# Optimization experiments

Hardware: AMD Instinct MI355X
Metric: run time of the kernel (lower is better)

Reference implementation:

```python
import jax, jax.numpy as jnp
import numpy as np

N, E, D, ED, H = 50000, 800000, 128, 16, 1
EPS = 1e-5


def setup_inputs() -> dict:
    key = jax.random.key(0)
    ks = jax.random.split(key, 12)
    return {
        "x": jax.random.normal(ks[0], (N, D), jnp.float32),
        "edge_index": jax.random.randint(ks[1], (2, E), 0, N),
        "edge_attr": jax.random.normal(ks[2], (E, ED), jnp.float32),
        # GATv2Conv params
        "W_l": jax.random.normal(ks[3], (D, H * D), jnp.float32) / np.sqrt(D),
        "b_l": jnp.zeros((H * D,), jnp.float32),
        "W_r": jax.random.normal(ks[4], (D, H * D), jnp.float32) / np.sqrt(D),
        "b_r": jnp.zeros((H * D,), jnp.float32),
        "W_e": jax.random.normal(ks[5], (ED, H * D), jnp.float32) / np.sqrt(ED),
        "att": jax.random.normal(ks[6], (H, D), jnp.float32) * 0.1,
        "bias_gat": jnp.zeros((D,), jnp.float32),
        # block params
        "weight1": jax.random.normal(ks[7], (2,), jnp.float32),
        "bn1_gamma": jnp.ones((D,), jnp.float32),
        "bn1_beta": jnp.zeros((D,), jnp.float32),
        "conv_w": jax.random.normal(ks[8], (D, D, 3), jnp.float32) / np.sqrt(3 * D),
        "conv_b": jnp.zeros((D,), jnp.float32),
        "weight2": jax.random.normal(ks[9], (2,), jnp.float32),
        "bn2_gamma": jnp.ones((D,), jnp.float32),
        "bn2_beta": jnp.zeros((D,), jnp.float32),
    }


def _batch_norm(z, gamma, beta):
    # NodeLevelBatchNorm in training mode: stats over all nodes of the batch graph
    mu = z.mean(axis=0)
    var = z.var(axis=0)
    return (z - mu) * jax.lax.rsqrt(var + EPS) * gamma + beta


def _gatv2(x, edge_index, edge_attr, W_l, b_l, W_r, b_r, W_e, att, bias_gat):
    n = x.shape[0]
    # add self loops with edge_attr fill_value=0
    loop = jnp.arange(n)
    src = jnp.concatenate([edge_index[0], loop])  # message sources j
    dst = jnp.concatenate([edge_index[1], loop])  # message targets i
    x_l = (x @ W_l + b_l).reshape(n, H, D)
    x_r = (x @ W_r + b_r).reshape(n, H, D)
    e = (edge_attr @ W_e).reshape(-1, H, D)
    e = jnp.concatenate([e, jnp.zeros((n, H, D), e.dtype)], axis=0)  # zeros: lin_edge(0)=0
    # [E+N, H, D] edge messages
    m = jax.nn.leaky_relu(x_l[src] + x_r[dst] + e, negative_slope=0.2)
    logits = jnp.einsum('ehc,hc->eh', m, att)  # [E+N, H]
    # softmax grouped by target node (every node has a self loop -> no empty segments)
    lmax = jax.ops.segment_max(logits, dst, num_segments=n)
    p = jnp.exp(logits - lmax[dst])
    denom = jax.ops.segment_sum(p, dst, num_segments=n)
    alpha = p / denom[dst]
    out = jax.ops.segment_sum(alpha[:, :, None] * x_l[src], dst, num_segments=n)  # [N,H,D]
    return out.mean(axis=1) + bias_gat  # concat=False -> head mean


def reference(x, edge_index, edge_attr, W_l, b_l, W_r, b_r, W_e, att, bias_gat,
              weight1, bn1_gamma, bn1_beta, conv_w, conv_b, weight2,
              bn2_gamma, bn2_beta):
    attn_feat = _gatv2(x, edge_index, edge_attr, W_l, b_l, W_r, b_r, W_e, att, bias_gat)
    w1 = jax.nn.softmax(weight1)
    z = w1[0] * x + w1[1] * attn_feat
    z = _batch_norm(z, bn1_gamma, bn1_beta)
    # Conv1d over the node dimension: [1, C, N] -> [1, C, N]
    z1 = jax.lax.conv_general_dilated(
        z.T[None], conv_w, window_strides=(1,), padding=[(1, 1)],
        dimension_numbers=('NCH', 'OIH', 'NCH'))
    z1 = z1[0].T + conv_b  # [N, C]
    z1 = jax.nn.leaky_relu(z1, negative_slope=0.01)  # dropout inactive in eval
    w2 = jax.nn.softmax(weight2)
    z = w2[0] * z + w2[1] * z1
    z = _batch_norm(z, bn2_gamma, bn2_beta)
    return z
```

## Files before the change

kernel.cpp:

```cpp
#include <hip/hip_runtime.h>
#include <hip/hip_bf16.h>
#include <math.h>

#define DD 128
#define EPSBN 1e-5f

typedef float f2 __attribute__((ext_vector_type(2)));

__device__ __forceinline__ float4 f4_add(float4 a, float4 b) {
    return make_float4(a.x + b.x, a.y + b.y, a.z + b.z, a.w + b.w);
}
__device__ __forceinline__ float4 f4_fma(float a, float4 b, float4 c) {
    c.x = fmaf(a, b.x, c.x); c.y = fmaf(a, b.y, c.y);
    c.z = fmaf(a, b.z, c.z); c.w = fmaf(a, b.w, c.w);
    return c;
}
__device__ __forceinline__ float leakyf(float v, float s) { return v > 0.f ? v : s * v; }

__device__ __forceinline__ unsigned short f2bf(float f) {
    unsigned u = __float_as_uint(f);
    return (unsigned short)((u + 0x7fffu + ((u >> 16) & 1u)) >> 16);
}
__device__ __forceinline__ f2 bfu2f2(unsigned u) {
    f2 r;
    r.x = __uint_as_float(u << 16);
    r.y = __uint_as_float(u & 0xFFFF0000u);
    return r;
}
__device__ __forceinline__ f2 leaky2(f2 v, float s) {
    f2 z = (f2)0.f;
    return __builtin_elementwise_max(v, z) + s * __builtin_elementwise_min(v, z);
}

__global__ __launch_bounds__(256) void k_prep(const float* __restrict__ conv_w, float* __restrict__ wT,
                                              int* __restrict__ counts, float* __restrict__ stats,
                                              int n, int nstats) {
    int idx = blockIdx.x * 256 + threadIdx.x;
    if (idx < 3 * 128 * 128) {
        int k = idx >> 14;
        int r = idx & 16383;
        int ci = r >> 7, co = r & 127;
        wT[idx] = conv_w[(size_t)co * 384 + ci * 3 + k];
    }
    int z = idx - 3 * 128 * 128;
    if (z >= 0) {
        if (z < n) counts[z] = 0;
        else if (z - n < nstats) stats[z - n] = 0.f;
    }
}

__global__ __launch_bounds__(256) void k_gemm_xlxr(
    const float* __restrict__ x, const float* __restrict__ Wl, const float* __restrict__ bl,
    const float* __restrict__ Wr, const float* __restrict__ br,
    float* __restrict__ XR, unsigned short* __restrict__ XLh, int n)
{
    __shared__ float As[64 * 33];
    __shared__ float Bs[32 * 256];
    int tid = threadIdx.x;
    int r0 = blockIdx.x * 64;
    int tx = tid & 31, ty = tid >> 5;

    float4 accL[8], accR[8];
    #pragma unroll
    for (int j = 0; j < 8; ++j) {
        accL[j] = make_float4(0.f, 0.f, 0.f, 0.f);
        accR[j] = make_float4(0.f, 0.f, 0.f, 0.f);
    }

    for (int k0 = 0; k0 < 128; k0 += 32) {
        for (int idx = tid; idx < 64 * 32; idx += 256) {
            int lrow = idx >> 5, kk = idx & 31;
            int g = r0 + lrow;
            As[lrow * 33 + kk] = (g < n) ? x[(size_t)g * DD + k0 + kk] : 0.f;
        }
        for (int idx = tid; idx < 2048; idx += 256) {
            int kk = idx >> 6, co4 = idx & 63;
            float4 v;
            if (co4 < 32) v = ((const float4*)Wl)[(size_t)(k0 + kk) * 32 + co4];
            else          v = ((const float4*)Wr)[(size_t)(k0 + kk) * 32 + (co4 - 32)];
            ((float4*)Bs)[kk * 64 + co4] = v;
        }
        __syncthreads();

        #pragma unroll 4
        for (int kk = 0; kk < 32; ++kk) {
            float a[8];
            #pragma unroll
            for (int j = 0; j < 8; ++j) a[j] = As[(ty * 8 + j) * 33 + kk];
            float4 bL = ((float4*)Bs)[kk * 64 + tx];
            float4 bR = ((float4*)Bs)[kk * 64 + 32 + tx];
            #pragma unroll
            for (int j = 0; j < 8; ++j) {
                accL[j] = f4_fma(a[j], bL, accL[j]);
                accR[j] = f4_fma(a[j], bR, accR[j]);
            }
        }
        __syncthreads();
    }

    float4 blv = ((const float4*)bl)[tx];
    float4 brv = ((const float4*)br)[tx];
    #pragma unroll
    for (int j = 0; j < 8; ++j) {
        int row = r0 + ty * 8 + j;
        if (row < n) {
            float4 L4 = f4_add(accL[j], blv);
            ((float4*)(XR + (size_t)row * DD))[tx] = f4_add(accR[j], brv);
            uint2 hp;
            hp.x = (unsigned)f2bf(L4.x) | ((unsigned)f2bf(L4.y) << 16);
            hp.y = (unsigned)f2bf(L4.z) | ((unsigned)f2bf(L4.w) << 16);
            ((uint2*)(XLh + (size_t)row * DD))[tx] = hp;
        }
    }
}

__global__ __launch_bounds__(256) void k_hist(const int* __restrict__ dst, int* __restrict__ counts, int e) {
    int idx = blockIdx.x * 256 + threadIdx.x;
    if (idx < e) atomicAdd(&counts[dst[idx]], 1);
}

__global__ __launch_bounds__(256) void k_scan1(const int* __restrict__ counts,
                                               int* __restrict__ offsets, int* __restrict__ bsum, int n) {
    __shared__ int tmp[256];
    int t = threadIdx.x;
    int i = blockIdx.x * 256 + t;
    int v = (i < n) ? counts[i] : 0;
    tmp[t] = v;
    __syncthreads();
    for (int off = 1; off < 256; off <<= 1) {
        int u = (t >= off) ? tmp[t - off] : 0;
        __syncthreads();
        tmp[t] += u;
        __syncthreads();
    }
    if (i < n) offsets[i] = tmp[t] - v;
    if (t == 255) bsum[blockIdx.x] = tmp[255];
}

__global__ __launch_bounds__(1024) void k_scan2(int* __restrict__ bsum, int nchunks) {
    __shared__ int tmp[1024];
    int t = threadIdx.x;
    int v = (t < nchunks) ? bsum[t] : 0;
    tmp[t] = v;
    __syncthreads();
    for (int off = 1; off < 1024; off <<= 1) {
        int u = (t >= off) ? tmp[t - off] : 0;
        __syncthreads();
        tmp[t] += u;
        __syncthreads();
    }
    if (t < nchunks) bsum[t] = tmp[t] - v;
    if (t == 0) bsum[nchunks] = tmp[nchunks - 1];
}

__global__ __launch_bounds__(256) void k_scan3(int* __restrict__ offsets, int* __restrict__ cursor,
                                               const int* __restrict__ bsum, int n, int nchunks) {
    int i = blockIdx.x * 256 + threadIdx.x;
    if (i < n) {
        int o = offsets[i] + bsum[i >> 8];
        offsets[i] = o;
        cursor[i] = o;
    }
    if (i == n) offsets[n] = bsum[nchunks];
}

__global__ __launch_bounds__(256) void k_scatter(const int* __restrict__ src, const int* __restrict__ dst,
                                                 int* __restrict__ cursor, int2* __restrict__ epair, int e) {
    int idx = blockIdx.x * 256 + threadIdx.x;
    if (idx >= e) return;
    int d = dst[idx];
    int pos = atomicAdd(&cursor[d], 1);
    epair[pos] = make_int2(idx, src[idx]);
}


#define EPROJ(EB_, J_, EV_) {                                                   \
    const float4* e4_ = ((const float4*)(EB_)) + (J_) * 4;                      \
    float4 a0_ = e4_[0], a1_ = e4_[1], a2_ = e4_[2], a3_ = e4_[3];              \
    f2 v_ = (f2)0.f;                                                            \
    v_ = __builtin_elementwise_fma((f2)a0_.x, w2[0],  v_);                      \
    v_ = __builtin_elementwise_fma((f2)a0_.y, w2[1],  v_);                      \
    v_ = __builtin_elementwise_fma((f2)a0_.z, w2[2],  v_);                      \
    v_ = __builtin_elementwise_fma((f2)a0_.w, w2[3],  v_);                      \
    v_ = __builtin_elementwise_fma((f2)a1_.x, w2[4],  v_);                      \
    v_ = __builtin_elementwise_fma((f2)a1_.y, w2[5],  v_);                      \
    v_ = __builtin_elementwise_fma((f2)a1_.z, w2[6],  v_);                      \
    v_ = __builtin_elementwise_fma((f2)a1_.w, w2[7],  v_);                      \
    v_ = __builtin_elementwise_fma((f2)a2_.x, w2[8],  v_);                      \
    v_ = __builtin_elementwise_fma((f2)a2_.y, w2[9],  v_);                      \
    v_ = __builtin_elementwise_fma((f2)a2_.z, w2[10], v_);                      \
    v_ = __builtin_elementwise_fma((f2)a2_.w, w2[11], v_);                      \
    v_ = __builtin_elementwise_fma((f2)a3_.x, w2[12], v_);                      \
    v_ = __builtin_elementwise_fma((f2)a3_.y, w2[13], v_);                      \
    v_ = __builtin_elementwise_fma((f2)a3_.z, w2[14], v_);                      \
    v_ = __builtin_elementwise_fma((f2)a3_.w, w2[15], v_);                      \
    EV_ = v_; }

#define GAT_LOAD4(q_, U0_, U1_, U2_, U3_, AV_) {                                \
    int2 g0_ = epair[q_], g1_ = epair[(q_) + 1];                                \
    int2 g2_ = epair[(q_) + 2], g3_ = epair[(q_) + 3];                          \
    int s0_ = __builtin_amdgcn_readfirstlane(g0_.y);                            \
    int s1_ = __builtin_amdgcn_readfirstlane(g1_.y);                            \
    int s2_ = __builtin_amdgcn_readfirstlane(g2_.y);                            \
    int s3_ = __builtin_amdgcn_readfirstlane(g3_.y);                            \
    U0_ = XLu[(size_t)s0_ * 64 + lane];                                         \
    U1_ = XLu[(size_t)s1_ * 64 + lane];                                         \
    U2_ = XLu[(size_t)s2_ * 64 + lane];                                         \
    U3_ = XLu[(size_t)s3_ * 64 + lane];                                         \
    int ej_ = esel == 0 ? g0_.x : esel == 1 ? g1_.x : esel == 2 ? g2_.x : g3_.x;\
    AV_ = edge_attr[(size_t)ej_ * 16 + ek]; }

#define GAT_COMPUTE4(U0_, U1_, U2_, U3_, EB_) {                                 \
    f2 x0_ = bfu2f2(U0_), x1_ = bfu2f2(U1_);                                    \
    f2 x2_ = bfu2f2(U2_), x3_ = bfu2f2(U3_);                                    \
    f2 ev0_, ev1_, ev2_, ev3_;                                                  \
    EPROJ(EB_, 0, ev0_); EPROJ(EB_, 1, ev1_);                                   \
    EPROJ(EB_, 2, ev2_); EPROJ(EB_, 3, ev3_);                                   \
    f2 m0_ = leaky2(x0_ + xr2 + ev0_, 0.2f);                                    \
    f2 m1_ = leaky2(x1_ + xr2 + ev1_, 0.2f);                                    \
    f2 m2_ = leaky2(x2_ + xr2 + ev2_, 0.2f);                                    \
    f2 m3_ = leaky2(x3_ + xr2 + ev3_, 0.2f);                                    \
    float l0_ = m0_.x * att2.x + m0_.y * att2.y;                                \
    float l1_ = m1_.x * att2.x + m1_.y * att2.y;                                \
    float l2_ = m2_.x * att2.x + m2_.y * att2.y;                                \
    float l3_ = m3_.x * att2.x + m3_.y * att2.y;                                \
    _Pragma("unroll")                                                           \
    for (int off_ = 32; off_ > 0; off_ >>= 1) {                                 \
        l0_ += __shfl_xor(l0_, off_, 64);                                       \
        l1_ += __shfl_xor(l1_, off_, 64);                                       \
        l2_ += __shfl_xor(l2_, off_, 64);                                       \
        l3_ += __shfl_xor(l3_, off_, 64);                                       \
    }                                                                           \
    float g0_ = __expf(l0_), g1_ = __expf(l1_);                                 \
    float g2_ = __expf(l2_), g3_ = __expf(l3_);                                 \
    S += (g0_ + g1_) + (g2_ + g3_);                                             \
    axy = __builtin_elementwise_fma((f2)g0_, x0_, axy);                         \
    axy = __builtin_elementwise_fma((f2)g1_, x1_, axy);                         \
    axy = __builtin_elementwise_fma((f2)g2_, x2_, axy);                         \
    axy = __builtin_elementwise_fma((f2)g3_, x3_, axy); }

__global__ __launch_bounds__(256) void k_gat(
    const unsigned short* __restrict__ XLh, const float* __restrict__ XR,
    const float* __restrict__ x,
    const int2* __restrict__ epair, const int* __restrict__ offsets,
    const float* __restrict__ edge_attr, const float* __restrict__ We,
    const float* __restrict__ att, const float* __restrict__ bias_gat,
    const float* __restrict__ weight1, float* __restrict__ Z, int n, int nwaves)
{
    __shared__ float ebuf[4][2][64];
    int wv   = threadIdx.x >> 6;
    int wid  = blockIdx.x * 4 + wv;
    int lane = threadIdx.x & 63;
    int c = lane * 2;
    int esel = lane >> 4, ek = lane & 15;
    const unsigned* __restrict__ XLu = (const unsigned*)XLh;
    float* ebA = &ebuf[wv][0][0];
    float* ebB = &ebuf[wv][1][0];

    f2 w2[16];
    #pragma unroll
    for (int k = 0; k < 16; ++k) w2[k] = *(const f2*)(We + k * DD + c);
    f2 att2 = *(const f2*)(att + c);
    f2 bg   = *(const f2*)(bias_gat + c);
    float w0 = weight1[0], w1v = weight1[1];
    float mw = fmaxf(w0, w1v);
    float e0w = __expf(w0 - mw), e1w = __expf(w1v - mw);
    float winv = 1.f / (e0w + e1w);
    float w1x = e0w * winv, w1a = e1w * winv;

    for (int i = wid; i < n; i += nwaves) {
        f2 xr2 = *(const f2*)(XR + (size_t)i * DD + c);
        f2 xli = bfu2f2(XLu[(size_t)i * 64 + lane]);

        f2 ms = leaky2(xli + xr2, 0.2f);
        float sl = ms.x * att2.x + ms.y * att2.y;
        #pragma unroll
        for (int off = 32; off > 0; off >>= 1) sl += __shfl_xor(sl, off, 64);
        float gs = __expf(sl);
        float S = gs;
        f2 axy = gs * xli;

        int p  = __builtin_amdgcn_readfirstlane(offsets[i]);
        int pe = __builtin_amdgcn_readfirstlane(offsets[i + 1]);
        int cnt = pe - p;
        int ng = cnt >> 2;

        if (ng > 0) {
            unsigned uA0, uA1, uA2, uA3, uB0, uB1, uB2, uB3;
            float avA, avB;
            GAT_LOAD4(p, uA0, uA1, uA2, uA3, avA);
            ebA[lane] = avA;
            int t = 0;
            for (;;) {
                bool mA = (t + 1 < ng);
                if (mA) GAT_LOAD4(p + 4 * (t + 1), uB0, uB1, uB2, uB3, avB);
                GAT_COMPUTE4(uA0, uA1, uA2, uA3, ebA);
                if (mA) ebB[lane] = avB;
                if (++t >= ng) break;
                bool mB = (t + 1 < ng);
                if (mB) GAT_LOAD4(p + 4 * (t + 1), uA0, uA1, uA2, uA3, avA);
                GAT_COMPUTE4(uB0, uB1, uB2, uB3, ebB);
                if (mB) ebA[lane] = avA;
                if (++t >= ng) break;
            }
        }
        for (int q = p + (ng << 2); q < pe; ++q) {
            int2 ej = epair[q];
            int eid = __builtin_amdgcn_readfirstlane(ej.x);
            int srn = __builtin_amdgcn_readfirstlane(ej.y);
            unsigned u = XLu[(size_t)srn * 64 + lane];
            const float* pa = edge_attr + (size_t)eid * 16;
            f2 ev = (f2)0.f;
            #pragma unroll
            for (int k = 0; k < 16; ++k) ev = __builtin_elementwise_fma((f2)pa[k], w2[k], ev);
            f2 x0 = bfu2f2(u);
            f2 m = leaky2(x0 + xr2 + ev, 0.2f);
            float l = m.x * att2.x + m.y * att2.y;
            #pragma unroll
            for (int off = 32; off > 0; off >>= 1) l += __shfl_xor(l, off, 64);
            float g = __expf(l);
            S += g;
            axy = __builtin_elementwise_fma((f2)g, x0, axy);
        }

        float rl = 1.f / S;
        f2 av = axy * rl + bg;
        f2 xv = *(const f2*)(x + (size_t)i * DD + c);
        f2 zv = w1x * xv + w1a * av;
        *(f2*)(Z + (size_t)i * DD + c) = zv;
    }
}

__global__ __launch_bounds__(256) void k_bn_stats(const float* __restrict__ Zin,
                                                  float* __restrict__ sums, float* __restrict__ sumsq, int n) {
    __shared__ float4 Ls[8][32];
    __shared__ float4 Lq[8][32];
    int tid = threadIdx.x;
    int cg = tid & 31, ry = tid >> 5;
    float4 s = make_float4(0.f, 0.f, 0.f, 0.f), q = s;
    for (int r = blockIdx.x * 8 + ry; r < n; r += gridDim.x * 8) {
        float4 v = ((const float4*)(Zin + (size_t)r * DD))[cg];
        s = f4_add(s, v);
        q.x = fmaf(v.x, v.x, q.x); q.y = fmaf(v.y, v.y, q.y);
        q.z = fmaf(v.z, v.z, q.z); q.w = fmaf(v.w, v.w, q.w);
    }
    Ls[ry][cg] = s; Lq[ry][cg] = q;
    __syncthreads();
    if (tid < 32) {
        float4 ts = Ls[0][tid], tq = Lq[0][tid];
        #pragma unroll
        for (int j = 1; j < 8; ++j) { ts = f4_add(ts, Ls[j][tid]); tq = f4_add(tq, Lq[j][tid]); }
        atomicAdd(&sums[tid * 4 + 0], ts.x); atomicAdd(&sums[tid * 4 + 1], ts.y);
        atomicAdd(&sums[tid * 4 + 2], ts.z); atomicAdd(&sums[tid * 4 + 3], ts.w);
        atomicAdd(&sumsq[tid * 4 + 0], tq.x); atomicAdd(&sumsq[tid * 4 + 1], tq.y);
        atomicAdd(&sumsq[tid * 4 + 2], tq.z); atomicAdd(&sumsq[tid * 4 + 3], tq.w);
    }
}

__global__ __launch_bounds__(128) void k_bn_finish(const float* __restrict__ sums, const float* __restrict__ sumsq,
                                                   const float* __restrict__ gamma, const float* __restrict__ beta,
                                                   float* __restrict__ scale, float* __restrict__ shift, int n) {
    int t = threadIdx.x;
    if (t >= 128) return;
    float fn = (float)n;
    float mu = sums[t] / fn;
    float var = sumsq[t] / fn - mu * mu;
    float rstd = rsqrtf(var + EPSBN);
    float sc = gamma[t] * rstd;
    scale[t] = sc;
    shift[t] = fmaf(-mu, sc, beta[t]);
}

__global__ __launch_bounds__(256) void k_conv(
    const float* __restrict__ Z, const float* __restrict__ scale1, const float* __restrict__ shift1,
    const float* __restrict__ wT, const float* __restrict__ conv_b,
    const float* __restrict__ weight2, float* __restrict__ Z2,
    float* __restrict__ sums2, float* __restrict__ sumsq2, int n)
{
    __shared__ float As[66 * 20];
    __shared__ float Bs[3 * 16 * 128];
    int tid = threadIdx.x;
    int r0 = blockIdx.x * 64;
    int tx = tid & 31, ty = tid >> 5;
    int rbase = ty * 8;

    float4 acc[8];
    #pragma unroll
    for (int j = 0; j < 8; ++j) acc[j] = make_float4(0.f, 0.f, 0.f, 0.f);

    f2 sc1c[2], sh1c[2];

    for (int ci0 = 0; ci0 < 128; ci0 += 16) {
        {
            int idx = tid;
            if (idx < 264) {
                int lrow = idx >> 2, c4 = (idx & 3) * 4;
                int g = r0 - 1 + lrow;
                int cc = ci0 + c4;
                float4 v = make_float4(0.f, 0.f, 0.f, 0.f);
                if (g >= 0 && g < n) {
                    float4 zv = *(const float4*)(Z + (size_t)g * DD + cc);
                    const float4 s4v = *(const float4*)(scale1 + cc);
                    const float4 h4v = *(const float4*)(shift1 + cc);
                    v.x = fmaf(zv.x, s4v.x, h4v.x); v.y = fmaf(zv.y, s4v.y, h4v.y);
                    v.z = fmaf(zv.z, s4v.z, h4v.z); v.w = fmaf(zv.w, s4v.w, h4v.w);
                }
                *(float4*)(As + lrow * 20 + c4) = v;
            }
            if (idx + 256 < 264) { }
            idx = tid + 256;
            if (idx < 264) {
                int lrow = idx >> 2, c4 = (idx & 3) * 4;
                int g = r0 - 1 + lrow;
                int cc = ci0 + c4;
                float4 v = make_float4(0.f, 0.f, 0.f, 0.f);
                if (g >= 0 && g < n) {
                    float4 zv = *(const float4*)(Z + (size_t)g * DD + cc);
                    const float4 s4v = *(const float4*)(scale1 + cc);
                    const float4 h4v = *(const float4*)(shift1 + cc);
                    v.x = fmaf(zv.x, s4v.x, h4v.x); v.y = fmaf(zv.y, s4v.y, h4v.y);
                    v.z = fmaf(zv.z, s4v.z, h4v.z); v.w = fmaf(zv.w, s4v.w, h4v.w);
                }
                *(float4*)(As + lrow * 20 + c4) = v;
            }
        }
        #pragma unroll
        for (int s = 0; s < 6; ++s) {
            int idx = s * 256 + tid;
            int k = idx >> 9;
            int r = idx & 511;
            int ci = r >> 5, co4 = r & 31;
            ((float4*)Bs)[idx] = ((const float4*)wT)[(size_t)k * 4096 + (ci0 + ci) * 32 + co4];
        }
        __syncthreads();

        #pragma unroll 2
        for (int ci = 0; ci < 16; ++ci) {
            float a[10];
            #pragma unroll
            for (int j = 0; j < 10; ++j) a[j] = As[(rbase + j) * 20 + ci];
            float4 b0 = ((float4*)Bs)[(0 * 16 + ci) * 32 + tx];
            float4 b1 = ((float4*)Bs)[(1 * 16 + ci) * 32 + tx];
            float4 b2 = ((float4*)Bs)[(2 * 16 + ci) * 32 + tx];
            #pragma unroll
            for (int j = 0; j < 8; ++j) {
                acc[j] = f4_fma(a[j],     b0, acc[j]);
                acc[j] = f4_fma(a[j + 1], b1, acc[j]);
                acc[j] = f4_fma(a[j + 2], b2, acc[j]);
            }
        }
        __syncthreads();
    }

    float w0 = weight2[0], w1v = weight2[1];
    float mw = fmaxf(w0, w1v);
    float e0 = __expf(w0 - mw), e1 = __expf(w1v - mw);
    float winv = 1.f / (e0 + e1);
    float w2x = e0 * winv, w2a = e1 * winv;

    float4 cb = ((const float4*)conv_b)[tx];
    float4 sc1 = ((const float4*)scale1)[tx];
    float4 sh1 = ((const float4*)shift1)[tx];
    float4 s4 = make_float4(0.f, 0.f, 0.f, 0.f), q4 = s4;
    #pragma unroll
    for (int j = 0; j < 8; ++j) {
        int row = r0 + rbase + j;
        if (row >= n) break;
        float4 z1 = f4_add(acc[j], cb);
        z1.x = leakyf(z1.x, 0.01f); z1.y = leakyf(z1.y, 0.01f);
        z1.z = leakyf(z1.z, 0.01f); z1.w = leakyf(z1.w, 0.01f);
        float4 zv = ((const float4*)(Z + (size_t)row * DD))[tx];
        float4 zbn;
        zbn.x = fmaf(zv.x, sc1.x, sh1.x); zbn.y = fmaf(zv.y, sc1.y, sh1.y);
        zbn.z = fmaf(zv.z, sc1.z, sh1.z); zbn.w = fmaf(zv.w, sc1.w, sh1.w);
        float4 o;
        o.x = w2x * zbn.x + w2a * z1.x; o.y = w2x * zbn.y + w2a * z1.y;
        o.z = w2x * zbn.z + w2a * z1.z; o.w = w2x * zbn.w + w2a * z1.w;
        ((float4*)(Z2 + (size_t)row * DD))[tx] = o;
        s4 = f4_add(s4, o);
        q4.x = fmaf(o.x, o.x, q4.x); q4.y = fmaf(o.y, o.y, q4.y);
        q4.z = fmaf(o.z, o.z, q4.z); q4.w = fmaf(o.w, o.w, q4.w);
    }

    float4* rs = (float4*)Bs;
    float4* rq = rs + 256;
    rs[ty * 32 + tx] = s4;
    rq[ty * 32 + tx] = q4;
    __syncthreads();
    if (tid < 32) {
        float4 ts = rs[tid], tq = rq[tid];
        #pragma unroll
        for (int j = 1; j < 8; ++j) { ts = f4_add(ts, rs[j * 32 + tid]); tq = f4_add(tq, rq[j * 32 + tid]); }
        atomicAdd(&sums2[tid * 4 + 0], ts.x); atomicAdd(&sums2[tid * 4 + 1], ts.y);
        atomicAdd(&sums2[tid * 4 + 2], ts.z); atomicAdd(&sums2[tid * 4 + 3], ts.w);
        atomicAdd(&sumsq2[tid * 4 + 0], tq.x); atomicAdd(&sumsq2[tid * 4 + 1], tq.y);
        atomicAdd(&sumsq2[tid * 4 + 2], tq.z); atomicAdd(&sumsq2[tid * 4 + 3], tq.w);
    }
}

__global__ __launch_bounds__(256) void k_final(const float* __restrict__ Z2,
                                               const float* __restrict__ scale2, const float* __restrict__ shift2,
                                               float* __restrict__ out, int total4) {
    int idx = blockIdx.x * 256 + threadIdx.x;
    if (idx >= total4) return;
    int c4 = idx & 31;
    float4 v = ((const float4*)Z2)[idx];
    float4 sc = ((const float4*)scale2)[c4];
    float4 sh = ((const float4*)shift2)[c4];
    float4 r;
    r.x = fmaf(v.x, sc.x, sh.x); r.y = fmaf(v.y, sc.y, sh.y);
    r.z = fmaf(v.z, sc.z, sh.z); r.w = fmaf(v.w, sc.w, sh.w);
    ((float4*)out)[idx] = r;
}

extern "C" void kernel_launch(void* const* d_in, const int* in_sizes, int n_in,
                              void* d_out, int out_size, void* d_ws, size_t ws_size,
                              hipStream_t stream)
{
    const float* x          = (const float*)d_in[0];
    const int*   edge_index = (const int*)d_in[1];
    const float* edge_attr  = (const float*)d_in[2];
    const float* W_l        = (const float*)d_in[3];
    const float* b_l        = (const float*)d_in[4];
    const float* W_r        = (const float*)d_in[5];
    const float* b_r        = (const float*)d_in[6];
    const float* W_e        = (const float*)d_in[7];
    const float* att        = (const float*)d_in[8];
    const float* bias_gat   = (const float*)d_in[9];
    const float* weight1    = (const float*)d_in[10];
    const float* bn1_gamma  = (const float*)d_in[11];
    const float* bn1_beta   = (const float*)d_in[12];
    const float* conv_w     = (const float*)d_in[13];
    const float* conv_b     = (const float*)d_in[14];
    const float* weight2    = (const float*)d_in[15];
    const float* bn2_gamma  = (const float*)d_in[16];
    const float* bn2_beta   = (const float*)d_in[17];

    int n = in_sizes[0] / DD;
    int e = in_sizes[1] / 2;
    int nchunks = (n + 255) / 256;

    float* XR = (float*)d_ws;
    float* Z  = XR + (size_t)n * DD;
    float* wT = Z + (size_t)n * DD;
    float* stats = wT + 49152;
    float* sums1 = stats,       *sumsq1 = stats + 128;
    float* sums2 = stats + 256, *sumsq2 = stats + 384;
    float* scale1 = stats + 512, *shift1 = stats + 640;
    float* scale2 = stats + 768, *shift2 = stats + 896;
    int* counts  = (int*)(stats + 1024);
    int* offsets = counts + n;
    int* cursor  = offsets + n + 2;
    int* bsum    = cursor + n;
    int2* epair  = (int2*)(bsum + ((nchunks + 2) & ~1));
    unsigned short* XLh = (unsigned short*)(epair + e);
    float* Z2 = XR;

    const int* src = edge_index;
    const int* dst = edge_index + e;

    const int nwaves = 8192;

    k_prep<<<(3 * 128 * 128 + n + 512 + 255) / 256, 256, 0, stream>>>(conv_w, wT, counts, stats, n, 512);
    k_gemm_xlxr<<<(n + 63) / 64, 256, 0, stream>>>(x, W_l, b_l, W_r, b_r, XR, XLh, n);
    k_hist<<<(e + 255) / 256, 256, 0, stream>>>(dst, counts, e);
    k_scan1<<<nchunks, 256, 0, stream>>>(counts, offsets, bsum, n);
    k_scan2<<<1, 1024, 0, stream>>>(bsum, nchunks);
    k_scan3<<<(n + 256) / 256, 256, 0, stream>>>(offsets, cursor, bsum, n, nchunks);
    k_scatter<<<(e + 255) / 256, 256, 0, stream>>>(src, dst, cursor, epair, e);
    k_gat<<<nwaves / 4, 256, 0, stream>>>(XLh, XR, x, epair, offsets,
                                          edge_attr, W_e, att, bias_gat, weight1, Z, n, nwaves);
    k_bn_stats<<<256, 256, 0, stream>>>(Z, sums1, sumsq1, n);
    k_bn_finish<<<1, 128, 0, stream>>>(sums1, sumsq1, bn1_gamma, bn1_beta, scale1, shift1, n);
    k_conv<<<(n + 63) / 64, 256, 0, stream>>>(Z, scale1, shift1, wT, conv_b, weight2, Z2,
                                              sums2, sumsq2, n);
    k_bn_finish<<<1, 128, 0, stream>>>(sums2, sumsq2, bn2_gamma, bn2_beta, scale2, shift2, n);
    k_final<<<(n * 32 + 255) / 256, 256, 0, stream>>>(Z2, scale2, shift2, (float*)d_out, n * 32);
}
```

Measured before the change: 578.1 us.

## Deepen GAT edge gather pipeline to three stages and pad tail groups

The GAT aggregation loop moves from double-buffered to triple-buffered prefetch of source-feature and edge-attribute groups, so loads run two groups ahead of compute. The scalar per-edge tail loop is removed. The last partial group of four is padded by clamping indices to the final edge and zeroing its exp weights. The conv tile load is also folded into a small unrolled loop, which is only a cleanup. In exchange the change raises register and LDS use and does wasted work on padded lanes.

New measurement: 581.8 us. About the same (+0.6%).

```diff
diff --git a/kernel.cpp b/kernel.cpp
--- a/kernel.cpp
+++ b/kernel.cpp
@@ -197,8 +197,11 @@
     EV_ = v_; }
 
 #define GAT_LOAD4(q_, U0_, U1_, U2_, U3_, AV_) {                                \
-    int2 g0_ = epair[q_], g1_ = epair[(q_) + 1];                                \
-    int2 g2_ = epair[(q_) + 2], g3_ = epair[(q_) + 3];                          \
+    int q1_ = (q_) + 1 < pe ? (q_) + 1 : pe - 1;                                \
+    int q2_ = (q_) + 2 < pe ? (q_) + 2 : pe - 1;                                \
+    int q3_ = (q_) + 3 < pe ? (q_) + 3 : pe - 1;                                \
+    int2 g0_ = epair[q_], g1_ = epair[q1_];                                     \
+    int2 g2_ = epair[q2_], g3_ = epair[q3_];                                    \
     int s0_ = __builtin_amdgcn_readfirstlane(g0_.y);                            \
     int s1_ = __builtin_amdgcn_readfirstlane(g1_.y);                            \
     int s2_ = __builtin_amdgcn_readfirstlane(g2_.y);                            \
@@ -210,7 +213,7 @@
     int ej_ = esel == 0 ? g0_.x : esel == 1 ? g1_.x : esel == 2 ? g2_.x : g3_.x;\
     AV_ = edge_attr[(size_t)ej_ * 16 + ek]; }
 
-#define GAT_COMPUTE4(U0_, U1_, U2_, U3_, EB_) {                                 \
+#define GAT_COMPUTE4(BQ_, U0_, U1_, U2_, U3_, EB_) {                            \
     f2 x0_ = bfu2f2(U0_), x1_ = bfu2f2(U1_);                                    \
     f2 x2_ = bfu2f2(U2_), x3_ = bfu2f2(U3_);                                    \
     f2 ev0_, ev1_, ev2_, ev3_;                                                  \
@@ -231,8 +234,10 @@
         l2_ += __shfl_xor(l2_, off_, 64);                                       \
         l3_ += __shfl_xor(l3_, off_, 64);                                       \
     }                                                                           \
-    float g0_ = __expf(l0_), g1_ = __expf(l1_);                                 \
-    float g2_ = __expf(l2_), g3_ = __expf(l3_);                                 \
+    float g0_ = (BQ_) + 0 < pe ? __expf(l0_) : 0.f;                             \
+    float g1_ = (BQ_) + 1 < pe ? __expf(l1_) : 0.f;                             \
+    float g2_ = (BQ_) + 2 < pe ? __expf(l2_) : 0.f;                             \
+    float g3_ = (BQ_) + 3 < pe ? __expf(l3_) : 0.f;                             \
     S += (g0_ + g1_) + (g2_ + g3_);                                             \
     axy = __builtin_elementwise_fma((f2)g0_, x0_, axy);                         \
     axy = __builtin_elementwise_fma((f2)g1_, x1_, axy);                         \
@@ -247,7 +252,7 @@
     const float* __restrict__ att, const float* __restrict__ bias_gat,
     const float* __restrict__ weight1, float* __restrict__ Z, int n, int nwaves)
 {
-    __shared__ float ebuf[4][2][64];
+    __shared__ float ebuf[4][3][64];
     int wv   = threadIdx.x >> 6;
     int wid  = blockIdx.x * 4 + wv;
     int lane = threadIdx.x & 63;
@@ -256,6 +261,7 @@
     const unsigned* __restrict__ XLu = (const unsigned*)XLh;
     float* ebA = &ebuf[wv][0][0];
     float* ebB = &ebuf[wv][1][0];
+    float* ebC = &ebuf[wv][2][0];
 
     f2 w2[16];
     #pragma unroll
@@ -283,44 +289,29 @@
         int p  = __builtin_amdgcn_readfirstlane(offsets[i]);
         int pe = __builtin_amdgcn_readfirstlane(offsets[i + 1]);
         int cnt = pe - p;
-        int ng = cnt >> 2;
+        int ng = (cnt + 3) >> 2;
 
         if (ng > 0) {
-            unsigned uA0, uA1, uA2, uA3, uB0, uB1, uB2, uB3;
-            float avA, avB;
+            unsigned uA0, uA1, uA2, uA3, uB0, uB1, uB2, uB3, uC0, uC1, uC2, uC3;
+            float avA, avB, avC;
             GAT_LOAD4(p, uA0, uA1, uA2, uA3, avA);
             ebA[lane] = avA;
+            if (ng > 1) GAT_LOAD4(p + 4, uB0, uB1, uB2, uB3, avB);
             int t = 0;
             for (;;) {
-                bool mA = (t + 1 < ng);
-                if (mA) GAT_LOAD4(p + 4 * (t + 1), uB0, uB1, uB2, uB3, avB);
-                GAT_COMPUTE4(uA0, uA1, uA2, uA3, ebA);
-                if (mA) ebB[lane] = avB;
+                if (t + 2 < ng) GAT_LOAD4(p + 4 * (t + 2), uC0, uC1, uC2, uC3, avC);
+                if (t + 1 < ng) ebB[lane] = avB;
+                GAT_COMPUTE4(p + 4 * t, uA0, uA1, uA2, uA3, ebA);
                 if (++t >= ng) break;
-                bool mB = (t + 1 < ng);
-                if (mB) GAT_LOAD4(p + 4 * (t + 1), uA0, uA1, uA2, uA3, avA);
-                GAT_COMPUTE4(uB0, uB1, uB2, uB3, ebB);
-                if (mB) ebA[lane] = avA;
+                if (t + 2 < ng) GAT_LOAD4(p + 4 * (t + 2), uA0, uA1, uA2, uA3, avA);
+                if (t + 1 < ng) ebC[lane] = avC;
+                GAT_COMPUTE4(p + 4 * t, uB0, uB1, uB2, uB3, ebB);
+                if (++t >= ng) break;
+                if (t + 2 < ng) GAT_LOAD4(p + 4 * (t + 2), uB0, uB1, uB2, uB3, avB);
+                if (t + 1 < ng) ebA[lane] = avA;
+                GAT_COMPUTE4(p + 4 * t, uC0, uC1, uC2, uC3, ebC);
                 if (++t >= ng) break;
             }
-        }
-        for (int q = p + (ng << 2); q < pe; ++q) {
-            int2 ej = epair[q];
-            int eid = __builtin_amdgcn_readfirstlane(ej.x);
-            int srn = __builtin_amdgcn_readfirstlane(ej.y);
-            unsigned u = XLu[(size_t)srn * 64 + lane];
-            const float* pa = edge_attr + (size_t)eid * 16;
-            f2 ev = (f2)0.f;
-            #pragma unroll
-            for (int k = 0; k < 16; ++k) ev = __builtin_elementwise_fma((f2)pa[k], w2[k], ev);
-            f2 x0 = bfu2f2(u);
-            f2 m = leaky2(x0 + xr2 + ev, 0.2f);
-            float l = m.x * att2.x + m.y * att2.y;
-            #pragma unroll
-            for (int off = 32; off > 0; off >>= 1) l += __shfl_xor(l, off, 64);
-            float g = __expf(l);
-            S += g;
-            axy = __builtin_elementwise_fma((f2)g, x0, axy);
         }
 
         float rl = 1.f / S;
@@ -388,27 +379,10 @@
     #pragma unroll
     for (int j = 0; j < 8; ++j) acc[j] = make_float4(0.f, 0.f, 0.f, 0.f);
 
-    f2 sc1c[2], sh1c[2];
-
     for (int ci0 = 0; ci0 < 128; ci0 += 16) {
-        {
-            int idx = tid;
-            if (idx < 264) {
-                int lrow = idx >> 2, c4 = (idx & 3) * 4;
-                int g = r0 - 1 + lrow;
-                int cc = ci0 + c4;
-                float4 v = make_float4(0.f, 0.f, 0.f, 0.f);
-                if (g >= 0 && g < n) {
-                    float4 zv = *(const float4*)(Z + (size_t)g * DD + cc);
-                    const float4 s4v = *(const float4*)(scale1 + cc);
-                    const float4 h4v = *(const float4*)(shift1 + cc);
-                    v.x = fmaf(zv.x, s4v.x, h4v.x); v.y = fmaf(zv.y, s4v.y, h4v.y);
-                    v.z = fmaf(zv.z, s4v.z, h4v.z); v.w = fmaf(zv.w, s4v.w, h4v.w);
-                }
-                *(float4*)(As + lrow * 20 + c4) = v;
-            }
-            if (idx + 256 < 264) { }
-            idx = tid + 256;
+        #pragma unroll
+        for (int s = 0; s < 2; ++s) {
+            int idx = s * 256 + tid;
             if (idx < 264) {
                 int lrow = idx >> 2, c4 = (idx & 3) * 4;
                 int g = r0 - 1 + lrow;
```
